# Performance work log

Hardware: AMD Instinct MI355X
Metric: run time of the kernel (lower is better)

## Reference

```python
import jax, jax.numpy as jnp
import numpy as np

H = W = 20  # module hardcodes visual_feature_map_h/w = 20
STAGES = 6
IN_POINTS = 36
HID = 256
B = 1024


def grid_sample_bilinear_border(fm, grid):
    """PyTorch-equivalent grid_sample, mode='bilinear', padding_mode='border',
    align_corners=False. fm: (B,C,H,W); grid: (B,P,2) in [-1,1] (x,y order).
    Returns (B,C,P)."""
    b, c, h, w = fm.shape
    # unnormalize (align_corners=False), then border-clip the coordinate
    x = jnp.clip((grid[..., 0] + 1.0) * w * 0.5 - 0.5, 0.0, w - 1.0)  # (B,P)
    y = jnp.clip((grid[..., 1] + 1.0) * h * 0.5 - 0.5, 0.0, h - 1.0)
    x0f = jnp.floor(x); y0f = jnp.floor(y)
    wx = (x - x0f)[:, None, :]  # (B,1,P)
    wy = (y - y0f)[:, None, :]
    x0 = x0f.astype(jnp.int32); y0 = y0f.astype(jnp.int32)
    x1 = jnp.minimum(x0 + 1, w - 1); y1 = jnp.minimum(y0 + 1, h - 1)
    fmf = fm.reshape(b, c, h * w)

    def gather(yi, xi):
        idx = (yi * w + xi)[:, None, :]  # (B,1,P)
        return jnp.take_along_axis(fmf, jnp.broadcast_to(idx, (b, c, idx.shape[-1])), axis=2)

    v00 = gather(y0, x0); v01 = gather(y0, x1)
    v10 = gather(y1, x0); v11 = gather(y1, x1)
    return (v00 * (1 - wx) * (1 - wy) + v01 * wx * (1 - wy)
            + v10 * (1 - wx) * wy + v11 * wx * wy)


def setup_inputs() -> dict:
    key = jax.random.key(0)
    ks = jax.random.split(key, 16)
    s = 0.02  # small param scale so sampled points stay mostly in-grid
    return {
        "sampling_query": jax.random.normal(ks[0], (B, HID), jnp.float32),
        "reference_point": jax.random.uniform(ks[1], (B, 2), jnp.float32),
        "feature_map": jax.random.normal(ks[2], (B, HID, H * W), jnp.float32),
        "pos": jax.random.normal(ks[3], (B, HID, H * W), jnp.float32),
        "offset_W": jax.random.normal(ks[4], (STAGES, IN_POINTS * 2, HID), jnp.float32) * s,
        "offset_b": jax.random.uniform(ks[5], (STAGES, IN_POINTS * 2), jnp.float32) - 0.5,
        "up_W1": jax.random.normal(ks[6], (STAGES, HID, 2 * HID), jnp.float32) * s,
        "up_b1": jax.random.normal(ks[7], (STAGES, HID), jnp.float32) * s,
        "up_W2": jax.random.normal(ks[8], (STAGES, HID, HID), jnp.float32) * s,
        "up_b2": jax.random.normal(ks[9], (STAGES, HID), jnp.float32) * s,
        "bbox_W1": jax.random.normal(ks[10], (HID, HID), jnp.float32) * s,
        "bbox_b1": jax.random.normal(ks[11], (HID,), jnp.float32) * s,
        "bbox_W2": jax.random.normal(ks[12], (HID, HID), jnp.float32) * s,
        "bbox_b2": jax.random.normal(ks[13], (HID,), jnp.float32) * s,
        "bbox_W3": jax.random.normal(ks[14], (4, HID), jnp.float32) * s,
        "bbox_b3": jax.random.normal(ks[15], (4,), jnp.float32) * s,
    }


def reference(sampling_query, reference_point, feature_map, pos,
              offset_W, offset_b, up_W1, up_b1, up_W2, up_b2,
              bbox_W1, bbox_b1, bbox_W2, bbox_b2, bbox_W3, bbox_b3):
    bs = sampling_query.shape[0]
    fm = feature_map.reshape(bs, HID, H, W)
    pm = pos.reshape(bs, HID, H, W)
    q = sampling_query
    for s in range(STAGES):  # fixed small stage count -> Python loop ok
        # offset generator: Linear(hidden -> in_points*2)
        xy = (q @ offset_W[s].T + offset_b[s]).reshape(bs, IN_POINTS, 2)
        pts = xy + reference_point[:, None, :]          # (B,P,2) in [0,1]
        grid = 2.0 * pts - 1.0                          # -> [-1,1]
        sampled = grid_sample_bilinear_border(fm, grid)  # (B,C,P)
        pe = grid_sample_bilinear_border(pm, grid)       # (B,C,P)
        fused = (sampled + pe).mean(axis=-1)             # (B,C) pooled over points
        # update_sampling_queries[s]: MLP(2*hidden -> hidden -> hidden)
        cat = jnp.concatenate([fused, q], axis=1)        # (B,2C)
        hdd = jax.nn.relu(cat @ up_W1[s].T + up_b1[s])
        q = hdd @ up_W2[s].T + up_b2[s]
    # bbox_embed: 3-layer MLP, relu on first two, sigmoid box
    hx = jax.nn.relu(q @ bbox_W1.T + bbox_b1)
    hx = jax.nn.relu(hx @ bbox_W2.T + bbox_b2)
    pred_box = jax.nn.sigmoid(hx @ bbox_W3.T + bbox_b3)  # (B,4)
    return pred_box
```

## Files before the change

### kernel.cpp

```cpp
#include <hip/hip_runtime.h>
#include <hip/hip_bf16.h>

#define B_SZ   1024
#define HIDN   256
#define NSTAGE 6
#define NPTS   36
#define HGT    20
#define WID    20
#define HW     400
#define MB     4
#define NTHR   1024

#define W_OFFW   0
#define W_UW1    110592
#define W_UW2    897024
#define W_BW1    1290240
#define W_BW2    1355776
#define W_TOTAL  1421312

static __device__ __forceinline__ unsigned int f2bf(float x) {
    unsigned int u = __float_as_uint(x);
    u += 0x7FFFu + ((u >> 16) & 1u);
    return u >> 16;
}
static __device__ __forceinline__ float bf2f(unsigned short h) {
    return __uint_as_float((unsigned int)h << 16);
}
static __device__ __forceinline__ float bflo(unsigned int u) {
    return __uint_as_float(u << 16);
}
static __device__ __forceinline__ float bfhi(unsigned int u) {
    return __uint_as_float(u & 0xFFFF0000u);
}

__global__ __launch_bounds__(256) void wconv_kernel(
    const float* __restrict__ offW, const float* __restrict__ uW1,
    const float* __restrict__ uW2,  const float* __restrict__ bW1,
    const float* __restrict__ bW2,  unsigned short* __restrict__ dst)
{
    int i = blockIdx.x * 256 + threadIdx.x;
    if (i >= W_TOTAL) return;
    float v;
    if (i < W_UW1)       v = offW[i - W_OFFW];
    else if (i < W_UW2)  v = uW1[i - W_UW1];
    else if (i < W_BW1)  v = uW2[i - W_UW2];
    else if (i < W_BW2)  v = bW1[i - W_BW1];
    else                 v = bW2[i - W_BW2];
    dst[i] = (unsigned short)f2bf(v);
}

__global__ __launch_bounds__(640) void prepass_kernel(
    const float* __restrict__ fm, const float* __restrict__ pos,
    unsigned short* __restrict__ fmp)
{
    const int b  = blockIdx.y;
    const int ct = blockIdx.x;
    __shared__ unsigned short tile[HW * 65];
    const int t = threadIdx.x;

    const size_t gbase = ((size_t)b * HIDN + ct * 64) * HW;
    #pragma unroll 1
    for (int k = 0; k < 5; ++k) {
        const int i0 = t + (2 * k) * 640;
        const int i1 = i0 + 640;
        const float4 a0 = *(const float4*)(fm  + gbase + 4 * (size_t)i0);
        const float4 q0 = *(const float4*)(pos + gbase + 4 * (size_t)i0);
        const float4 a1 = *(const float4*)(fm  + gbase + 4 * (size_t)i1);
        const float4 q1 = *(const float4*)(pos + gbase + 4 * (size_t)i1);
        const int c0 = i0 / 100, k40 = i0 - c0 * 100;
        const int c1 = i1 / 100, k41 = i1 - c1 * 100;
        tile[(4 * k40 + 0) * 65 + c0] = (unsigned short)f2bf(a0.x + q0.x);
        tile[(4 * k40 + 1) * 65 + c0] = (unsigned short)f2bf(a0.y + q0.y);
        tile[(4 * k40 + 2) * 65 + c0] = (unsigned short)f2bf(a0.z + q0.z);
        tile[(4 * k40 + 3) * 65 + c0] = (unsigned short)f2bf(a0.w + q0.w);
        tile[(4 * k41 + 0) * 65 + c1] = (unsigned short)f2bf(a1.x + q1.x);
        tile[(4 * k41 + 1) * 65 + c1] = (unsigned short)f2bf(a1.y + q1.y);
        tile[(4 * k41 + 2) * 65 + c1] = (unsigned short)f2bf(a1.z + q1.z);
        tile[(4 * k41 + 3) * 65 + c1] = (unsigned short)f2bf(a1.w + q1.w);
    }
    __syncthreads();

    const int u2 = t & 31;
    const int h0 = t >> 5;
    uint* outp = (uint*)(fmp + (((size_t)b * 4 + ct) * HW) * 64);
    #pragma unroll
    for (int w = 0; w < 20; ++w) {
        const int hw = h0 + 20 * w;
        const unsigned int lo = tile[hw * 65 + 2 * u2 + 0];
        const unsigned int hi = tile[hw * 65 + 2 * u2 + 1];
        outp[(size_t)hw * 32 + u2] = lo | (hi << 16);
    }
}

template <int K, int O, int ACT>
__device__ __forceinline__ void gemm_v3(
    const float* __restrict__ W, const float* __restrict__ bias,
    const float* __restrict__ i0, const float* __restrict__ i1,
    const float* __restrict__ i2, const float* __restrict__ i3,
    float* __restrict__ o0, float* __restrict__ o1,
    float* __restrict__ o2, float* __restrict__ o3,
    int kp, int og)
{
    const float4* p0 = (const float4*)i0;
    const float4* p1 = (const float4*)i1;
    const float4* p2 = (const float4*)i2;
    const float4* p3 = (const float4*)i3;
    #pragma unroll
    for (int pass = 0; pass < (O + 127) / 128; ++pass) {
        const int o = pass * 128 + og;
        float a0 = 0.f, a1 = 0.f, a2 = 0.f, a3 = 0.f;
        if (o < O) {
            const float4* wr = (const float4*)(W + (size_t)o * K);
            #pragma unroll 4
            for (int jj = 0; jj < K / 32; ++jj) {
                const int j = kp + 8 * jj;
                const float4 w  = wr[j];
                const float4 v0 = p0[j];
                const float4 v1 = p1[j];
                const float4 v2 = p2[j];
                const float4 v3 = p3[j];
                a0 += w.x * v0.x + w.y * v0.y + w.z * v0.z + w.w * v0.w;
                a1 += w.x * v1.x + w.y * v1.y + w.z * v1.z + w.w * v1.w;
                a2 += w.x * v2.x + w.y * v2.y + w.z * v2.z + w.w * v2.w;
                a3 += w.x * v3.x + w.y * v3.y + w.z * v3.z + w.w * v3.w;
            }
        }
        a0 += __shfl_xor(a0, 1); a0 += __shfl_xor(a0, 2); a0 += __shfl_xor(a0, 4);
        a1 += __shfl_xor(a1, 1); a1 += __shfl_xor(a1, 2); a1 += __shfl_xor(a1, 4);
        a2 += __shfl_xor(a2, 1); a2 += __shfl_xor(a2, 2); a2 += __shfl_xor(a2, 4);
        a3 += __shfl_xor(a3, 1); a3 += __shfl_xor(a3, 2); a3 += __shfl_xor(a3, 4);
        if (kp == 0 && o < O) {
            const float bz = bias[o];
            float r0 = a0 + bz, r1 = a1 + bz, r2 = a2 + bz, r3 = a3 + bz;
            if (ACT == 1) {
                r0 = fmaxf(r0, 0.f); r1 = fmaxf(r1, 0.f);
                r2 = fmaxf(r2, 0.f); r3 = fmaxf(r3, 0.f);
            }
            if (ACT == 2) {
                r0 = 1.f / (1.f + expf(-r0)); r1 = 1.f / (1.f + expf(-r1));
                r2 = 1.f / (1.f + expf(-r2)); r3 = 1.f / (1.f + expf(-r3));
            }
            o0[o] = r0; o1[o] = r1; o2[o] = r2; o3[o] = r3;
        }
    }
}

template <int K, int O, int ACT>
__device__ __forceinline__ void gemm_bf(
    const unsigned short* __restrict__ W, const float* __restrict__ bias,
    const float* __restrict__ i0, const float* __restrict__ i1,
    const float* __restrict__ i2, const float* __restrict__ i3,
    float* __restrict__ o0, float* __restrict__ o1,
    float* __restrict__ o2, float* __restrict__ o3,
    int kp, int og)
{
    const float4* p0 = (const float4*)i0;
    const float4* p1 = (const float4*)i1;
    const float4* p2 = (const float4*)i2;
    const float4* p3 = (const float4*)i3;
    #pragma unroll
    for (int pass = 0; pass < (O + 127) / 128; ++pass) {
        const int o = pass * 128 + og;
        float a0 = 0.f, a1 = 0.f, a2 = 0.f, a3 = 0.f;
        if (o < O) {
            const uint2* wr = (const uint2*)(W + (size_t)o * K);
            #pragma unroll 4
            for (int jj = 0; jj < K / 32; ++jj) {
                const int j = kp + 8 * jj;
                const uint2 wq = wr[j];
                const float w0 = bflo(wq.x), w1 = bfhi(wq.x);
                const float w2 = bflo(wq.y), w3 = bfhi(wq.y);
                const float4 v0 = p0[j];
                const float4 v1 = p1[j];
                const float4 v2 = p2[j];
                const float4 v3 = p3[j];
                a0 += w0 * v0.x + w1 * v0.y + w2 * v0.z + w3 * v0.w;
                a1 += w0 * v1.x + w1 * v1.y + w2 * v1.z + w3 * v1.w;
                a2 += w0 * v2.x + w1 * v2.y + w2 * v2.z + w3 * v2.w;
                a3 += w0 * v3.x + w1 * v3.y + w2 * v3.z + w3 * v3.w;
            }
        }
        a0 += __shfl_xor(a0, 1); a0 += __shfl_xor(a0, 2); a0 += __shfl_xor(a0, 4);
        a1 += __shfl_xor(a1, 1); a1 += __shfl_xor(a1, 2); a1 += __shfl_xor(a1, 4);
        a2 += __shfl_xor(a2, 1); a2 += __shfl_xor(a2, 2); a2 += __shfl_xor(a2, 4);
        a3 += __shfl_xor(a3, 1); a3 += __shfl_xor(a3, 2); a3 += __shfl_xor(a3, 4);
        if (kp == 0 && o < O) {
            const float bz = bias[o];
            float r0 = a0 + bz, r1 = a1 + bz, r2 = a2 + bz, r3 = a3 + bz;
            if (ACT == 1) {
                r0 = fmaxf(r0, 0.f); r1 = fmaxf(r1, 0.f);
                r2 = fmaxf(r2, 0.f); r3 = fmaxf(r3, 0.f);
            }
            if (ACT == 2) {
                r0 = 1.f / (1.f + expf(-r0)); r1 = 1.f / (1.f + expf(-r1));
                r2 = 1.f / (1.f + expf(-r2)); r3 = 1.f / (1.f + expf(-r3));
            }
            o0[o] = r0; o1[o] = r1; o2[o] = r2; o3[o] = r3;
        }
    }
}

__global__ __launch_bounds__(NTHR) void mdetr6_kernel(
    const float* __restrict__ q_in,  const float* __restrict__ refpt,
    const unsigned short* __restrict__ fmp,
    const unsigned short* __restrict__ offWb, const float* __restrict__ offB,
    const unsigned short* __restrict__ uW1b,  const float* __restrict__ uB1,
    const unsigned short* __restrict__ uW2b,  const float* __restrict__ uB2,
    const unsigned short* __restrict__ bW1b,  const float* __restrict__ bb1,
    const unsigned short* __restrict__ bW2b,  const float* __restrict__ bb2,
    const float* __restrict__ bW3,   const float* __restrict__ bb3,
    float* __restrict__ out)
{
    const int b0 = blockIdx.x * MB;
    const int t  = threadIdx.x;
    const int kp = t & 7;
    const int og = t >> 3;

    __shared__ __attribute__((aligned(16))) float cat_s[MB][2 * HIDN];
    __shared__ __attribute__((aligned(16))) float hdd_s[MB][HIDN];
    __shared__ __attribute__((aligned(16))) float xy_s[MB][80];
    __shared__ __attribute__((aligned(16))) float wgt_s[MB][144];
    __shared__ __attribute__((aligned(16))) int   off_s[MB][144];

    {
        const int m = t >> 8, c = t & 255;
        cat_s[m][HIDN + c] = q_in[(size_t)(b0 + m) * HIDN + c];
    }

    for (int s = 0; s < NSTAGE; ++s) {
        __syncthreads();
        gemm_bf<HIDN, NPTS * 2, 0>(
            offWb + (size_t)s * NPTS * 2 * HIDN, offB + s * NPTS * 2,
            cat_s[0] + HIDN, cat_s[1] + HIDN, cat_s[2] + HIDN, cat_s[3] + HIDN,
            xy_s[0], xy_s[1], xy_s[2], xy_s[3], kp, og);
        __syncthreads();
        if (t < MB * NPTS) {
            const int m = t / NPTS, p = t % NPTS;
            const int bm = b0 + m;
            float px = xy_s[m][2 * p + 0] + refpt[2 * bm + 0];
            float py = xy_s[m][2 * p + 1] + refpt[2 * bm + 1];
            float x = fminf(fmaxf(px * (float)WID - 0.5f, 0.f), (float)(WID - 1));
            float y = fminf(fmaxf(py * (float)HGT - 0.5f, 0.f), (float)(HGT - 1));
            float x0f = floorf(x), y0f = floorf(y);
            float wx = x - x0f,   wy = y - y0f;
            int x0 = (int)x0f, y0 = (int)y0f;
            int x1 = min(x0 + 1, WID - 1), y1 = min(y0 + 1, HGT - 1);
            const float inv = 1.f / (float)NPTS;
            wgt_s[m][4 * p + 0] = (1.f - wx) * (1.f - wy) * inv;
            wgt_s[m][4 * p + 1] = wx * (1.f - wy) * inv;
            wgt_s[m][4 * p + 2] = (1.f - wx) * wy * inv;
            wgt_s[m][4 * p + 3] = wx * wy * inv;
            off_s[m][4 * p + 0] = (y0 * WID + x0) * 64;
            off_s[m][4 * p + 1] = (y0 * WID + x1) * 64;
            off_s[m][4 * p + 2] = (y1 * WID + x0) * 64;
            off_s[m][4 * p + 3] = (y1 * WID + x1) * 64;
        }
        __syncthreads();
        {
            const int m = t >> 8, c = t & 255;
            const unsigned short* base =
                fmp + (((size_t)(b0 + m) * 4 + (c >> 6)) * HW) * 64 + (c & 63);
            float acc = 0.f;
            #pragma unroll 6
            for (int p = 0; p < NPTS; ++p) {
                const int4   o4 = ((const int4*)off_s[m])[p];
                const float4 w4 = ((const float4*)wgt_s[m])[p];
                acc += w4.x * bf2f(base[o4.x]) + w4.y * bf2f(base[o4.y])
                     + w4.z * bf2f(base[o4.z]) + w4.w * bf2f(base[o4.w]);
            }
            cat_s[m][c] = acc;
        }
        __syncthreads();
        gemm_bf<2 * HIDN, HIDN, 1>(
            uW1b + (size_t)s * HIDN * 2 * HIDN, uB1 + s * HIDN,
            cat_s[0], cat_s[1], cat_s[2], cat_s[3],
            hdd_s[0], hdd_s[1], hdd_s[2], hdd_s[3], kp, og);
        __syncthreads();
        gemm_bf<HIDN, HIDN, 0>(
            uW2b + (size_t)s * HIDN * HIDN, uB2 + s * HIDN,
            hdd_s[0], hdd_s[1], hdd_s[2], hdd_s[3],
            cat_s[0] + HIDN, cat_s[1] + HIDN, cat_s[2] + HIDN, cat_s[3] + HIDN,
            kp, og);
    }
    __syncthreads();
    gemm_bf<HIDN, HIDN, 1>(bW1b, bb1,
        cat_s[0] + HIDN, cat_s[1] + HIDN, cat_s[2] + HIDN, cat_s[3] + HIDN,
        hdd_s[0], hdd_s[1], hdd_s[2], hdd_s[3], kp, og);
    __syncthreads();
    gemm_bf<HIDN, HIDN, 1>(bW2b, bb2,
        hdd_s[0], hdd_s[1], hdd_s[2], hdd_s[3],
        cat_s[0], cat_s[1], cat_s[2], cat_s[3], kp, og);
    __syncthreads();
    gemm_v3<HIDN, 4, 2>(bW3, bb3,
        cat_s[0], cat_s[1], cat_s[2], cat_s[3],
        out + (size_t)(b0 + 0) * 4, out + (size_t)(b0 + 1) * 4,
        out + (size_t)(b0 + 2) * 4, out + (size_t)(b0 + 3) * 4, kp, og);
}

__global__ __launch_bounds__(256) void mdetr_direct_kernel(
    const float* __restrict__ q_in,  const float* __restrict__ refpt,
    const float* __restrict__ fm,    const float* __restrict__ pos,
    const float* __restrict__ offW,  const float* __restrict__ offB,
    const float* __restrict__ uW1,   const float* __restrict__ uB1,
    const float* __restrict__ uW2,   const float* __restrict__ uB2,
    const float* __restrict__ bW1,   const float* __restrict__ bb1,
    const float* __restrict__ bW2,   const float* __restrict__ bb2,
    const float* __restrict__ bW3,   const float* __restrict__ bb3,
    float* __restrict__ out)
{
    const int b = blockIdx.x;
    const int t = threadIdx.x;
    __shared__ __attribute__((aligned(16))) float q_s[HIDN];
    __shared__ __attribute__((aligned(16))) float fused_s[HIDN];
    __shared__ __attribute__((aligned(16))) float hdd_s[HIDN];
    __shared__ float xy_s[NPTS * 2];
    __shared__ int   off_s[NPTS * 4];
    __shared__ float w_s[NPTS * 4];

    q_s[t] = q_in[(size_t)b * HIDN + t];
    const float rpx = refpt[2 * b + 0];
    const float rpy = refpt[2 * b + 1];

    for (int s = 0; s < NSTAGE; ++s) {
        __syncthreads();
        if (t < NPTS * 2) {
            const float4* wrow = (const float4*)(offW + ((size_t)s * 72 + t) * HIDN);
            const float4* q4   = (const float4*)q_s;
            float a0 = 0.f;
            #pragma unroll 8
            for (int k = 0; k < HIDN / 4; ++k) {
                float4 w4 = wrow[k]; float4 qq = q4[k];
                a0 += w4.x * qq.x + w4.y * qq.y + w4.z * qq.z + w4.w * qq.w;
            }
            xy_s[t] = offB[s * 72 + t] + a0;
        }
        __syncthreads();
        if (t < NPTS) {
            float px = xy_s[2 * t + 0] + rpx;
            float py = xy_s[2 * t + 1] + rpy;
            float x = fminf(fmaxf(px * (float)WID - 0.5f, 0.f), (float)(WID - 1));
            float y = fminf(fmaxf(py * (float)HGT - 0.5f, 0.f), (float)(HGT - 1));
            float x0f = floorf(x), y0f = floorf(y);
            float wx = x - x0f, wy = y - y0f;
            int x0 = (int)x0f, y0 = (int)y0f;
            int x1 = min(x0 + 1, WID - 1), y1 = min(y0 + 1, HGT - 1);
            const float inv = 1.f / (float)NPTS;
            w_s[4 * t + 0] = (1.f - wx) * (1.f - wy) * inv;
            w_s[4 * t + 1] = wx * (1.f - wy) * inv;
            w_s[4 * t + 2] = (1.f - wx) * wy * inv;
            w_s[4 * t + 3] = wx * wy * inv;
            off_s[4 * t + 0] = y0 * WID + x0;
            off_s[4 * t + 1] = y0 * WID + x1;
            off_s[4 * t + 2] = y1 * WID + x0;
            off_s[4 * t + 3] = y1 * WID + x1;
        }
        __syncthreads();
        {
            float acc = 0.f;
            const float* basef = fm  + ((size_t)b * HIDN + t) * HW;
            const float* basep = pos + ((size_t)b * HIDN + t) * HW;
            #pragma unroll 6
            for (int p = 0; p < NPTS; ++p)
                for (int k = 0; k < 4; ++k) {
                    int idx = off_s[4 * p + k];
                    acc += w_s[4 * p + k] * (basef[idx] + basep[idx]);
                }
            fused_s[t] = acc;
        }
        __syncthreads();
        {
            const float4* w1 = (const float4*)(uW1 + ((size_t)s * HIDN + t) * (2 * HIDN));
            const float4* f4 = (const float4*)fused_s;
            const float4* q4 = (const float4*)q_s;
            float a0 = 0.f;
            #pragma unroll 8
            for (int k = 0; k < HIDN / 4; ++k) {
                float4 w4 = w1[k]; float4 c4 = f4[k];
                a0 += w4.x * c4.x + w4.y * c4.y + w4.z * c4.z + w4.w * c4.w;
            }
            #pragma unroll 8
            for (int k = 0; k < HIDN / 4; ++k) {
                float4 w4 = w1[HIDN / 4 + k]; float4 c4 = q4[k];
                a0 += w4.x * c4.x + w4.y * c4.y + w4.z * c4.z + w4.w * c4.w;
            }
            hdd_s[t] = fmaxf(uB1[s * HIDN + t] + a0, 0.f);
        }
        __syncthreads();
        {
            const float4* w2 = (const float4*)(uW2 + ((size_t)s * HIDN + t) * HIDN);
            const float4* h4 = (const float4*)hdd_s;
            float a0 = 0.f;
            #pragma unroll 8
            for (int k = 0; k < HIDN / 4; ++k) {
                float4 w4 = w2[k]; float4 c4 = h4[k];
                a0 += w4.x * c4.x + w4.y * c4.y + w4.z * c4.z + w4.w * c4.w;
            }
            q_s[t] = uB2[s * HIDN + t] + a0;
        }
    }
    __syncthreads();
    {
        const float4* w = (const float4*)(bW1 + (size_t)t * HIDN);
        const float4* q4 = (const float4*)q_s;
        float a0 = 0.f;
        #pragma unroll 8
        for (int k = 0; k < HIDN / 4; ++k) {
            float4 w4 = w[k]; float4 c4 = q4[k];
            a0 += w4.x * c4.x + w4.y * c4.y + w4.z * c4.z + w4.w * c4.w;
        }
        hdd_s[t] = fmaxf(bb1[t] + a0, 0.f);
    }
    __syncthreads();
    {
        const float4* w = (const float4*)(bW2 + (size_t)t * HIDN);
        const float4* h4 = (const float4*)hdd_s;
        float a0 = 0.f;
        #pragma unroll 8
        for (int k = 0; k < HIDN / 4; ++k) {
            float4 w4 = w[k]; float4 c4 = h4[k];
            a0 += w4.x * c4.x + w4.y * c4.y + w4.z * c4.z + w4.w * c4.w;
        }
        fused_s[t] = fmaxf(bb2[t] + a0, 0.f);
    }
    __syncthreads();
    if (t < 4) {
        const float* w = bW3 + (size_t)t * HIDN;
        float h = bb3[t];
        #pragma unroll 16
        for (int k = 0; k < HIDN; ++k) h += w[k] * fused_s[k];
        out[(size_t)b * 4 + t] = 1.f / (1.f + expf(-h));
    }
}

extern "C" void kernel_launch(void* const* d_in, const int* in_sizes, int n_in,
                              void* d_out, int out_size, void* d_ws, size_t ws_size,
                              hipStream_t stream)
{
    const float* q    = (const float*)d_in[0];
    const float* rp   = (const float*)d_in[1];
    const float* fm   = (const float*)d_in[2];
    const float* pos  = (const float*)d_in[3];
    const float* offW = (const float*)d_in[4];
    const float* offB = (const float*)d_in[5];
    const float* uW1  = (const float*)d_in[6];
    const float* uB1  = (const float*)d_in[7];
    const float* uW2  = (const float*)d_in[8];
    const float* uB2  = (const float*)d_in[9];
    const float* bW1  = (const float*)d_in[10];
    const float* bb1  = (const float*)d_in[11];
    const float* bW2  = (const float*)d_in[12];
    const float* bb2  = (const float*)d_in[13];
    const float* bW3  = (const float*)d_in[14];
    const float* bb3  = (const float*)d_in[15];
    float* out = (float*)d_out;

    const size_t fmp_elems = (size_t)B_SZ * HW * HIDN;
    const size_t need = (fmp_elems + W_TOTAL) * sizeof(unsigned short);
    if (ws_size >= need) {
        unsigned short* fmp = (unsigned short*)d_ws;
        unsigned short* wbf = fmp + fmp_elems;
        wconv_kernel<<<W_TOTAL / 256, 256, 0, stream>>>(offW, uW1, uW2, bW1, bW2, wbf);
        prepass_kernel<<<dim3(4, B_SZ), 640, 0, stream>>>(fm, pos, fmp);
        mdetr6_kernel<<<B_SZ / MB, NTHR, 0, stream>>>(
            q, rp, fmp,
            wbf + W_OFFW, offB, wbf + W_UW1, uB1, wbf + W_UW2, uB2,
            wbf + W_BW1, bb1, wbf + W_BW2, bb2, bW3, bb3, out);
    } else {
        mdetr_direct_kernel<<<B_SZ, 256, 0, stream>>>(
            q, rp, fm, pos, offW, offB, uW1, uB1, uW2, uB2,
            bW1, bb1, bW2, bb2, bW3, bb3, out);
    }
}
```

Before: 350.0 us.

## Halve batch rows per block and split point sampling across thread halves

Each block now handles 2 batch rows instead of 4, which doubles the grid to 512 blocks so the GPU's compute units are better filled. To keep all 1024 threads busy during sampling, the 36 points are split into two halves of 18. Each half accumulates a partial sum, and the two are added through a new shared buffer. The trade-off is that each block now reuses its weight loads across only 2 rows instead of 4, so total weight traffic from L2 roughly doubles. There is also one extra barrier per stage.

```diff
diff --git a/kernel.cpp b/kernel.cpp
--- a/kernel.cpp
+++ b/kernel.cpp
@@ -8,7 +8,7 @@
 #define HGT    20
 #define WID    20
 #define HW     400
-#define MB     4
+#define MB     2
 #define NTHR   1024
 
 #define W_OFFW   0
@@ -93,22 +93,18 @@
 }
 
 template <int K, int O, int ACT>
-__device__ __forceinline__ void gemm_v3(
+__device__ __forceinline__ void gemm_f2(
     const float* __restrict__ W, const float* __restrict__ bias,
     const float* __restrict__ i0, const float* __restrict__ i1,
-    const float* __restrict__ i2, const float* __restrict__ i3,
     float* __restrict__ o0, float* __restrict__ o1,
-    float* __restrict__ o2, float* __restrict__ o3,
     int kp, int og)
 {
     const float4* p0 = (const float4*)i0;
     const float4* p1 = (const float4*)i1;
-    const float4* p2 = (const float4*)i2;
-    const float4* p3 = (const float4*)i3;
     #pragma unroll
     for (int pass = 0; pass < (O + 127) / 128; ++pass) {
         const int o = pass * 128 + og;
-        float a0 = 0.f, a1 = 0.f, a2 = 0.f, a3 = 0.f;
+        float a0 = 0.f, a1 = 0.f;
         if (o < O) {
             const float4* wr = (const float4*)(W + (size_t)o * K);
             #pragma unroll 4
@@ -117,51 +113,37 @@
                 const float4 w  = wr[j];
                 const float4 v0 = p0[j];
                 const float4 v1 = p1[j];
-                const float4 v2 = p2[j];
-                const float4 v3 = p3[j];
                 a0 += w.x * v0.x + w.y * v0.y + w.z * v0.z + w.w * v0.w;
                 a1 += w.x * v1.x + w.y * v1.y + w.z * v1.z + w.w * v1.w;
-                a2 += w.x * v2.x + w.y * v2.y + w.z * v2.z + w.w * v2.w;
-                a3 += w.x * v3.x + w.y * v3.y + w.z * v3.z + w.w * v3.w;
             }
         }
         a0 += __shfl_xor(a0, 1); a0 += __shfl_xor(a0, 2); a0 += __shfl_xor(a0, 4);
         a1 += __shfl_xor(a1, 1); a1 += __shfl_xor(a1, 2); a1 += __shfl_xor(a1, 4);
-        a2 += __shfl_xor(a2, 1); a2 += __shfl_xor(a2, 2); a2 += __shfl_xor(a2, 4);
-        a3 += __shfl_xor(a3, 1); a3 += __shfl_xor(a3, 2); a3 += __shfl_xor(a3, 4);
         if (kp == 0 && o < O) {
             const float bz = bias[o];
-            float r0 = a0 + bz, r1 = a1 + bz, r2 = a2 + bz, r3 = a3 + bz;
-            if (ACT == 1) {
-                r0 = fmaxf(r0, 0.f); r1 = fmaxf(r1, 0.f);
-                r2 = fmaxf(r2, 0.f); r3 = fmaxf(r3, 0.f);
-            }
+            float r0 = a0 + bz, r1 = a1 + bz;
+            if (ACT == 1) { r0 = fmaxf(r0, 0.f); r1 = fmaxf(r1, 0.f); }
             if (ACT == 2) {
                 r0 = 1.f / (1.f + expf(-r0)); r1 = 1.f / (1.f + expf(-r1));
-                r2 = 1.f / (1.f + expf(-r2)); r3 = 1.f / (1.f + expf(-r3));
-            }
-            o0[o] = r0; o1[o] = r1; o2[o] = r2; o3[o] = r3;
+            }
+            o0[o] = r0; o1[o] = r1;
         }
     }
 }
 
 template <int K, int O, int ACT>
-__device__ __forceinline__ void gemm_bf(
+__device__ __forceinline__ void gemm_bf2(
     const unsigned short* __restrict__ W, const float* __restrict__ bias,
     const float* __restrict__ i0, const float* __restrict__ i1,
-    const float* __restrict__ i2, const float* __restrict__ i3,
     float* __restrict__ o0, float* __restrict__ o1,
-    float* __restrict__ o2, float* __restrict__ o3,
     int kp, int og)
 {
     const float4* p0 = (const float4*)i0;
     const float4* p1 = (const float4*)i1;
-    const float4* p2 = (const float4*)i2;
-    const float4* p3 = (const float4*)i3;
     #pragma unroll
     for (int pass = 0; pass < (O + 127) / 128; ++pass) {
         const int o = pass * 128 + og;
-        float a0 = 0.f, a1 = 0.f, a2 = 0.f, a3 = 0.f;
+        float a0 = 0.f, a1 = 0.f;
         if (o < O) {
             const uint2* wr = (const uint2*)(W + (size_t)o * K);
             #pragma unroll 4
@@ -172,35 +154,25 @@
                 const float w2 = bflo(wq.y), w3 = bfhi(wq.y);
                 const float4 v0 = p0[j];
                 const float4 v1 = p1[j];
-                const float4 v2 = p2[j];
-                const float4 v3 = p3[j];
                 a0 += w0 * v0.x + w1 * v0.y + w2 * v0.z + w3 * v0.w;
                 a1 += w0 * v1.x + w1 * v1.y + w2 * v1.z + w3 * v1.w;
-                a2 += w0 * v2.x + w1 * v2.y + w2 * v2.z + w3 * v2.w;
-                a3 += w0 * v3.x + w1 * v3.y + w2 * v3.z + w3 * v3.w;
             }
         }
         a0 += __shfl_xor(a0, 1); a0 += __shfl_xor(a0, 2); a0 += __shfl_xor(a0, 4);
         a1 += __shfl_xor(a1, 1); a1 += __shfl_xor(a1, 2); a1 += __shfl_xor(a1, 4);
-        a2 += __shfl_xor(a2, 1); a2 += __shfl_xor(a2, 2); a2 += __shfl_xor(a2, 4);
-        a3 += __shfl_xor(a3, 1); a3 += __shfl_xor(a3, 2); a3 += __shfl_xor(a3, 4);
         if (kp == 0 && o < O) {
             const float bz = bias[o];
-            float r0 = a0 + bz, r1 = a1 + bz, r2 = a2 + bz, r3 = a3 + bz;
-            if (ACT == 1) {
-                r0 = fmaxf(r0, 0.f); r1 = fmaxf(r1, 0.f);
-                r2 = fmaxf(r2, 0.f); r3 = fmaxf(r3, 0.f);
-            }
+            float r0 = a0 + bz, r1 = a1 + bz;
+            if (ACT == 1) { r0 = fmaxf(r0, 0.f); r1 = fmaxf(r1, 0.f); }
             if (ACT == 2) {
                 r0 = 1.f / (1.f + expf(-r0)); r1 = 1.f / (1.f + expf(-r1));
-                r2 = 1.f / (1.f + expf(-r2)); r3 = 1.f / (1.f + expf(-r3));
-            }
-            o0[o] = r0; o1[o] = r1; o2[o] = r2; o3[o] = r3;
-        }
-    }
-}
-
-__global__ __launch_bounds__(NTHR) void mdetr6_kernel(
+            }
+            o0[o] = r0; o1[o] = r1;
+        }
+    }
+}
+
+__global__ __launch_bounds__(NTHR, 8) void mdetr7_kernel(
     const float* __restrict__ q_in,  const float* __restrict__ refpt,
     const unsigned short* __restrict__ fmp,
     const unsigned short* __restrict__ offWb, const float* __restrict__ offB,
@@ -218,21 +190,21 @@
 
     __shared__ __attribute__((aligned(16))) float cat_s[MB][2 * HIDN];
     __shared__ __attribute__((aligned(16))) float hdd_s[MB][HIDN];
+    __shared__ __attribute__((aligned(16))) float part_s[MB][2][HIDN];
     __shared__ __attribute__((aligned(16))) float xy_s[MB][80];
     __shared__ __attribute__((aligned(16))) float wgt_s[MB][144];
     __shared__ __attribute__((aligned(16))) int   off_s[MB][144];
 
-    {
+    if (t < MB * HIDN) {
         const int m = t >> 8, c = t & 255;
         cat_s[m][HIDN + c] = q_in[(size_t)(b0 + m) * HIDN + c];
     }
 
     for (int s = 0; s < NSTAGE; ++s) {
         __syncthreads();
-        gemm_bf<HIDN, NPTS * 2, 0>(
+        gemm_bf2<HIDN, NPTS * 2, 0>(
             offWb + (size_t)s * NPTS * 2 * HIDN, offB + s * NPTS * 2,
-            cat_s[0] + HIDN, cat_s[1] + HIDN, cat_s[2] + HIDN, cat_s[3] + HIDN,
-            xy_s[0], xy_s[1], xy_s[2], xy_s[3], kp, og);
+            cat_s[0] + HIDN, cat_s[1] + HIDN, xy_s[0], xy_s[1], kp, og);
         __syncthreads();
         if (t < MB * NPTS) {
             const int m = t / NPTS, p = t % NPTS;
@@ -257,44 +229,46 @@
         }
         __syncthreads();
         {
-            const int m = t >> 8, c = t & 255;
+            const int m = t >> 9;
+            const int h = (t >> 8) & 1;
+            const int c = t & 255;
             const unsigned short* base =
                 fmp + (((size_t)(b0 + m) * 4 + (c >> 6)) * HW) * 64 + (c & 63);
             float acc = 0.f;
+            const int p0 = 18 * h;
             #pragma unroll 6
-            for (int p = 0; p < NPTS; ++p) {
+            for (int p = p0; p < p0 + 18; ++p) {
                 const int4   o4 = ((const int4*)off_s[m])[p];
                 const float4 w4 = ((const float4*)wgt_s[m])[p];
                 acc += w4.x * bf2f(base[o4.x]) + w4.y * bf2f(base[o4.y])
                      + w4.z * bf2f(base[o4.z]) + w4.w * bf2f(base[o4.w]);
             }
-            cat_s[m][c] = acc;
-        }
-        __syncthreads();
-        gemm_bf<2 * HIDN, HIDN, 1>(
+            part_s[m][h][c] = acc;
+        }
+        __syncthreads();
+        if (t < MB * HIDN) {
+            const int m = t >> 8, c = t & 255;
+            cat_s[m][c] = part_s[m][0][c] + part_s[m][1][c];
+        }
+        __syncthreads();
+        gemm_bf2<2 * HIDN, HIDN, 1>(
             uW1b + (size_t)s * HIDN * 2 * HIDN, uB1 + s * HIDN,
-            cat_s[0], cat_s[1], cat_s[2], cat_s[3],
-            hdd_s[0], hdd_s[1], hdd_s[2], hdd_s[3], kp, og);
-        __syncthreads();
-        gemm_bf<HIDN, HIDN, 0>(
+            cat_s[0], cat_s[1], hdd_s[0], hdd_s[1], kp, og);
+        __syncthreads();
+        gemm_bf2<HIDN, HIDN, 0>(
             uW2b + (size_t)s * HIDN * HIDN, uB2 + s * HIDN,
-            hdd_s[0], hdd_s[1], hdd_s[2], hdd_s[3],
-            cat_s[0] + HIDN, cat_s[1] + HIDN, cat_s[2] + HIDN, cat_s[3] + HIDN,
-            kp, og);
-    }
-    __syncthreads();
-    gemm_bf<HIDN, HIDN, 1>(bW1b, bb1,
-        cat_s[0] + HIDN, cat_s[1] + HIDN, cat_s[2] + HIDN, cat_s[3] + HIDN,
-        hdd_s[0], hdd_s[1], hdd_s[2], hdd_s[3], kp, og);
-    __syncthreads();
-    gemm_bf<HIDN, HIDN, 1>(bW2b, bb2,
-        hdd_s[0], hdd_s[1], hdd_s[2], hdd_s[3],
-        cat_s[0], cat_s[1], cat_s[2], cat_s[3], kp, og);
-    __syncthreads();
-    gemm_v3<HIDN, 4, 2>(bW3, bb3,
-        cat_s[0], cat_s[1], cat_s[2], cat_s[3],
-        out + (size_t)(b0 + 0) * 4, out + (size_t)(b0 + 1) * 4,
-        out + (size_t)(b0 + 2) * 4, out + (size_t)(b0 + 3) * 4, kp, og);
+            hdd_s[0], hdd_s[1], cat_s[0] + HIDN, cat_s[1] + HIDN, kp, og);
+    }
+    __syncthreads();
+    gemm_bf2<HIDN, HIDN, 1>(bW1b, bb1,
+        cat_s[0] + HIDN, cat_s[1] + HIDN, hdd_s[0], hdd_s[1], kp, og);
+    __syncthreads();
+    gemm_bf2<HIDN, HIDN, 1>(bW2b, bb2,
+        hdd_s[0], hdd_s[1], cat_s[0], cat_s[1], kp, og);
+    __syncthreads();
+    gemm_f2<HIDN, 4, 2>(bW3, bb3,
+        cat_s[0], cat_s[1],
+        out + (size_t)(b0 + 0) * 4, out + (size_t)(b0 + 1) * 4, kp, og);
 }
 
 __global__ __launch_bounds__(256) void mdetr_direct_kernel(
@@ -461,7 +435,7 @@
         unsigned short* wbf = fmp + fmp_elems;
         wconv_kernel<<<W_TOTAL / 256, 256, 0, stream>>>(offW, uW1, uW2, bW1, bW2, wbf);
         prepass_kernel<<<dim3(4, B_SZ), 640, 0, stream>>>(fm, pos, fmp);
-        mdetr6_kernel<<<B_SZ / MB, NTHR, 0, stream>>>(
+        mdetr7_kernel<<<B_SZ / MB, NTHR, 0, stream>>>(
             q, rp, fmp,
             wbf + W_OFFW, offB, wbf + W_UW1, uB1, wbf + W_UW2, uB2,
             wbf + W_BW1, bb1, wbf + W_BW2, bb2, bW3, bb3, out);
```

New measurement: 447.9 us. +28.0%, slower.
